# Optimization experiments

Measured on AMD Instinct MI355X. Metric: run time of the kernel, lower is better.

## Reference

```python
import jax, jax.numpy as jnp
import numpy as np

N, T, C = 100000, 12, 32  # nodes, periods, hidden (A3TGCN out_channels hardcoded 32)
E = 3_200_000


def setup_inputs() -> dict:
    key = jax.random.key(0)
    ks = jax.random.split(key, 20)
    s_g = 1.0 / np.sqrt(1.0)        # GCNConv glorot-ish for in=1
    s_l = 1.0 / np.sqrt(2.0 * C)    # torch Linear default for in=2C
    s_h = 1.0 / np.sqrt(C)
    u = lambda k, shape, s: jax.random.uniform(k, shape, jnp.float32, -s, s)
    return {
        "x": jax.random.normal(ks[0], (N, T), jnp.float32),
        "edge_index": jax.random.randint(ks[1], (2, E), 0, N, jnp.int32),
        "edge_weight": jax.random.uniform(ks[2], (E,), jnp.float32),
        # TGCN gate GCNConv params (in_channels=1, out=C)
        "w_z": u(ks[3], (1, C), s_g), "b_z": jnp.zeros((C,), jnp.float32),
        "w_r": u(ks[4], (1, C), s_g), "b_r": jnp.zeros((C,), jnp.float32),
        "w_h": u(ks[5], (1, C), s_g), "b_h": jnp.zeros((C,), jnp.float32),
        # TGCN gate Linear params (torch layout [out=C, in=2C])
        "lw_z": u(ks[6], (C, 2 * C), s_l), "lb_z": u(ks[7], (C,), s_l),
        "lw_r": u(ks[8], (C, 2 * C), s_l), "lb_r": u(ks[9], (C,), s_l),
        "lw_h": u(ks[10], (C, 2 * C), s_l), "lb_h": u(ks[11], (C,), s_l),
        # A3TGCN temporal attention
        "att": jax.random.uniform(ks[12], (T,), jnp.float32),
        # head Linear(32, 1)
        "head_w": u(ks[13], (1, C), s_h), "head_b": u(ks[14], (1,), s_h),
    }


def reference(x, edge_index, edge_weight, w_z, b_z, w_r, b_r, w_h, b_h,
              lw_z, lb_z, lw_r, lb_r, lw_h, lb_h, att, head_w, head_b):
    n = x.shape[0]
    # --- GCN normalization with self-loops (fill value 1) ---
    loop = jnp.arange(n)
    s = jnp.concatenate([edge_index[0], loop])
    d = jnp.concatenate([edge_index[1], loop])
    w = jnp.concatenate([edge_weight, jnp.ones((n,), edge_weight.dtype)])
    deg = jax.ops.segment_sum(w, d, num_segments=n)
    dinv = jnp.where(deg > 0, jax.lax.rsqrt(deg), 0.0)
    norm = dinv[s] * w * dinv[d]
    # --- shared sparse aggregation: A_hat @ X for all periods at once ---
    # in_channels = 1, so GCNConv(X_t) = (A_hat x_t) * W + b; aggregate scalars [N,T]
    agg = jax.ops.segment_sum(norm[:, None] * x[s], d, num_segments=n)  # [N, T]
    # gate convolutions, [N, T, C]
    cz = agg[:, :, None] * w_z[0] + b_z
    ch = agg[:, :, None] * w_h[0] + b_h
    # A3TGCN passes H=None every period -> hidden starts at 0 each step, so
    # linear([conv, H]) reduces to conv @ W[:, :C].T + b, and the reset gate R
    # multiplies H=0 (no effect on output).
    Z = jax.nn.sigmoid(jnp.einsum('ntc,oc->nto', cz, lw_z[:, :C]) + lb_z)
    Ht = jnp.tanh(jnp.einsum('ntc,oc->nto', ch, lw_h[:, :C]) + lb_h)
    Hp = (1.0 - Z) * Ht  # per-period hidden state, [N, T, C]
    probs = jax.nn.softmax(att)
    h = jnp.einsum('t,ntc->nc', probs, Hp)  # attention-weighted temporal sum
    h = jax.nn.relu(h)
    return h @ head_w.T + head_b  # [N, 1]
```

## Files before the change

kernel.cpp:

```cpp
#include <hip/hip_runtime.h>

#define N_NODES 100000
#define T_P 12
#define C_H 32
#define E_EDGES 3200000

#define NODES_PER_B 128
#define NB 782
#define MAX_BE 5120

#define VEC_E (E_EDGES / 4)
#define P1_THREADS 512
#define P1_VECS 2048
#define NBLK1 ((VEC_E + P1_VECS - 1) / P1_VECS)


__global__ void params_kernel(const float* __restrict__ wz, const float* __restrict__ bz,
                              const float* __restrict__ wh, const float* __restrict__ bh,
                              const float* __restrict__ lwz, const float* __restrict__ lbz,
                              const float* __restrict__ lwh, const float* __restrict__ lbh,
                              const float* __restrict__ att, float* __restrict__ P,
                              int* __restrict__ cursor) {
    int o = threadIdx.x;
    if (o < NB) cursor[o] = 0;
    if (o < C_H) {
        float az = 0.f, bzv = 0.f, ah = 0.f, bhv = 0.f;
        for (int c = 0; c < C_H; ++c) {
            float lz = lwz[o * 2 * C_H + c];
            float lh = lwh[o * 2 * C_H + c];
            az += wz[c] * lz;  bzv += bz[c] * lz;
            ah += wh[c] * lh;  bhv += bh[c] * lh;
        }
        P[16 + o]  = az;  P[48 + o]  = bzv + lbz[o];
        P[80 + o]  = ah;  P[112 + o] = bhv + lbh[o];
    }
    if (o == 0) {
        float m = -1e30f;
        for (int t = 0; t < T_P; ++t) m = fmaxf(m, att[t]);
        float e[T_P], s = 0.f;
        for (int t = 0; t < T_P; ++t) { e[t] = __expf(att[t] - m); s += e[t]; }
        float inv = 1.0f / s;
        for (int t = 0; t < T_P; ++t) P[t] = e[t] * inv;
    }
}

__global__ void bucket_scatter_kernel(const int* __restrict__ src, const int* __restrict__ dst,
                                      const float* __restrict__ w, int* __restrict__ cursor,
                                      float2* __restrict__ entries) {
    __shared__ int h[NB];
    __shared__ int claim[NB];
    for (int i = threadIdx.x; i < NB; i += P1_THREADS) h[i] = 0;
    __syncthreads();
    const int4* d4 = (const int4*)dst;
    int vbase = blockIdx.x * P1_VECS;
    int4 dc[4];
    int4 rk[4];
#pragma unroll
    for (int k = 0; k < 4; ++k) {
        int v = vbase + threadIdx.x + k * P1_THREADS;
        if (v < VEC_E) {
            int4 d = d4[v];
            dc[k] = d;
            rk[k].x = atomicAdd(&h[d.x >> 7], 1);
            rk[k].y = atomicAdd(&h[d.y >> 7], 1);
            rk[k].z = atomicAdd(&h[d.z >> 7], 1);
            rk[k].w = atomicAdd(&h[d.w >> 7], 1);
        }
    }
    __syncthreads();
    for (int i = threadIdx.x; i < NB; i += P1_THREADS) {
        int c = h[i];
        claim[i] = c ? atomicAdd(&cursor[i], c) : 0;
    }
    __syncthreads();
    const int4* s4 = (const int4*)src;
    const float4* w4 = (const float4*)w;
#pragma unroll
    for (int k = 0; k < 4; ++k) {
        int v = vbase + threadIdx.x + k * P1_THREADS;
        if (v < VEC_E) {
            int4 s = s4[v];
            float4 ww = w4[v];
            int4 d = dc[k];
            int bin, dl, pos;
            bin = d.x >> 7; dl = d.x & 127;
            pos = bin * MAX_BE + claim[bin] + rk[k].x;
            entries[pos] = make_float2(__int_as_float(s.x | (dl << 17)), ww.x);
            bin = d.y >> 7; dl = d.y & 127;
            pos = bin * MAX_BE + claim[bin] + rk[k].y;
            entries[pos] = make_float2(__int_as_float(s.y | (dl << 17)), ww.y);
            bin = d.z >> 7; dl = d.z & 127;
            pos = bin * MAX_BE + claim[bin] + rk[k].z;
            entries[pos] = make_float2(__int_as_float(s.z | (dl << 17)), ww.z);
            bin = d.w >> 7; dl = d.w & 127;
            pos = bin * MAX_BE + claim[bin] + rk[k].w;
            entries[pos] = make_float2(__int_as_float(s.w | (dl << 17)), ww.w);
        }
    }
}

__global__ void __launch_bounds__(1024)
reorder_kernel(float2* __restrict__ entries, const int* __restrict__ cursor,
               int* __restrict__ node_off, int* __restrict__ node_end,
               float* __restrict__ dinv) {
    __shared__ float2 stage[MAX_BE];
    __shared__ int   cnt[NODES_PER_B];
    __shared__ float wsum[NODES_PER_B];
    __shared__ int   off[NODES_PER_B];
    __shared__ int   rnk[NODES_PER_B];
    int tid = threadIdx.x;
    int b = blockIdx.x;
    int lo = b * MAX_BE;
    int ne = cursor[b];
    if (ne > MAX_BE) ne = MAX_BE;
    if (tid < NODES_PER_B) { cnt[tid] = 0; wsum[tid] = 0.f; }
    __syncthreads();
    for (int k = tid; k < ne; k += 1024) {
        float2 e = entries[lo + k];
        stage[k] = e;
        int dl = (__float_as_int(e.x) >> 17) & 127;
        atomicAdd(&cnt[dl], 1);
        atomicAdd(&wsum[dl], e.y);
    }
    __syncthreads();
    if (tid < NODES_PER_B) off[tid] = cnt[tid];
    __syncthreads();
    for (int d = 1; d < NODES_PER_B; d <<= 1) {
        int t = (tid >= d && tid < NODES_PER_B) ? off[tid - d] : 0;
        __syncthreads();
        if (tid < NODES_PER_B) off[tid] += t;
        __syncthreads();
    }
    if (tid < NODES_PER_B) {
        int ex = off[tid] - cnt[tid];
        rnk[tid] = ex;
        int n = (b << 7) + tid;
        if (n < N_NODES) {
            node_off[n] = lo + ex;
            node_end[n] = lo + ex + cnt[tid];
            dinv[n] = rsqrtf(1.0f + wsum[tid]);
        }
    }
    __syncthreads();
    for (int k = tid; k < ne; k += 1024) {
        float2 e = stage[k];
        int u = __float_as_int(e.x);
        int dl = (u >> 17) & 127;
        int s = u & 0x1FFFF;
        int r = atomicAdd(&rnk[dl], 1);
        entries[lo + r] = make_float2(__int_as_float(s), e.y);
    }
}

__global__ void y_kernel(const float* __restrict__ x, const float* __restrict__ dinv,
                         float* __restrict__ y) {
    int n = blockIdx.x * blockDim.x + threadIdx.x;
    if (n >= N_NODES) return;
    float din = dinv[n];
    const float4* xn = (const float4*)(x + (size_t)n * T_P);
    float4 a0 = xn[0], a1 = xn[1], a2 = xn[2];
    a0.x *= din; a0.y *= din; a0.z *= din; a0.w *= din;
    a1.x *= din; a1.y *= din; a1.z *= din; a1.w *= din;
    a2.x *= din; a2.y *= din; a2.z *= din; a2.w *= din;
    float4* yn = (float4*)(y + ((size_t)n << 4));
    yn[0] = a0; yn[1] = a1; yn[2] = a2;
    yn[3] = make_float4(0.f, 0.f, 0.f, 0.f);
}

__global__ void __launch_bounds__(512, 8)
gather_final_kernel(const int* __restrict__ node_off, const int* __restrict__ node_end,
                    const float2* __restrict__ entries, const float* __restrict__ dinv,
                    const float* __restrict__ y, const float* __restrict__ P,
                    const float* __restrict__ head_w, const float* __restrict__ head_b,
                    float* __restrict__ out) {
    __shared__ float Ps[160];
    __shared__ float hws[32];
    if (threadIdx.x < 160) Ps[threadIdx.x] = P[threadIdx.x];
    if (threadIdx.x < 32) hws[threadIdx.x] = head_w[threadIdx.x];
    __syncthreads();
    int tid = blockIdx.x * blockDim.x + threadIdx.x;
    int n = tid >> 2;
    int lane = tid & 3;
    if (n >= N_NODES) return;
    int b = node_off[n], e = node_end[n];
    const float4* yn = (const float4*)(y + ((size_t)n << 4));
    float4 a0 = make_float4(0.f, 0.f, 0.f, 0.f);
    float4 a1 = a0, a2 = a0;
    if (lane == 0)      a0 = yn[0];
    else if (lane == 1) a1 = yn[1];
    else if (lane == 2) a2 = yn[2];
    for (int i = b + lane; i < e; i += 4) {
        float2 ent = entries[i];
        int s = __float_as_int(ent.x);
        float c = ent.y;
        const float4* ys = (const float4*)(y + ((size_t)s << 4));
        float4 s0 = ys[0], s1 = ys[1], s2 = ys[2];
        a0.x += c * s0.x; a0.y += c * s0.y; a0.z += c * s0.z; a0.w += c * s0.w;
        a1.x += c * s1.x; a1.y += c * s1.y; a1.z += c * s1.z; a1.w += c * s1.w;
        a2.x += c * s2.x; a2.y += c * s2.y; a2.z += c * s2.z; a2.w += c * s2.w;
    }
#define RED4(v) v += __shfl_xor(v, 1); v += __shfl_xor(v, 2)
    RED4(a0.x); RED4(a0.y); RED4(a0.z); RED4(a0.w);
    RED4(a1.x); RED4(a1.y); RED4(a1.z); RED4(a1.w);
    RED4(a2.x); RED4(a2.y); RED4(a2.z); RED4(a2.w);
#undef RED4
    float din = dinv[n];
    float av[T_P];
    av[0] = a0.x * din; av[1] = a0.y * din; av[2]  = a0.z * din; av[3]  = a0.w * din;
    av[4] = a1.x * din; av[5] = a1.y * din; av[6]  = a1.z * din; av[7]  = a1.w * din;
    av[8] = a2.x * din; av[9] = a2.y * din; av[10] = a2.z * din; av[11] = a2.w * din;
    float acc = 0.f;
#pragma unroll
    for (int k = 0; k < 8; ++k) {
        int c = (lane << 3) + k;
        float Az = Ps[16 + c], Bz = Ps[48 + c], Ah = Ps[80 + c], Bh = Ps[112 + c];
        float hc = 0.f;
#pragma unroll
        for (int t = 0; t < T_P; ++t) {
            float a = av[t];
            float oz = 1.f / (1.f + __expf(a * Az + Bz));
            float vv = a * Ah + Bh;
            float th = 1.f - 2.f / (1.f + __expf(2.f * vv));
            hc += Ps[t] * oz * th;
        }
        acc += fmaxf(hc, 0.f) * hws[c];
    }
    acc += __shfl_xor(acc, 1);
    acc += __shfl_xor(acc, 2);
    if (lane == 0) out[n] = acc + head_b[0];
}

extern "C" void kernel_launch(void* const* d_in, const int* in_sizes, int n_in,
                              void* d_out, int out_size, void* d_ws, size_t ws_size,
                              hipStream_t stream) {
    const float* x    = (const float*)d_in[0];
    const int*   ei   = (const int*)d_in[1];
    const float* ew   = (const float*)d_in[2];
    const float* w_z  = (const float*)d_in[3];
    const float* b_z  = (const float*)d_in[4];
    const float* w_h  = (const float*)d_in[7];
    const float* b_h  = (const float*)d_in[8];
    const float* lw_z = (const float*)d_in[9];
    const float* lb_z = (const float*)d_in[10];
    const float* lw_h = (const float*)d_in[13];
    const float* lb_h = (const float*)d_in[14];
    const float* att  = (const float*)d_in[15];
    const float* hw   = (const float*)d_in[16];
    const float* hb   = (const float*)d_in[17];
    float* out = (float*)d_out;

    float* wsf      = (float*)d_ws;
    float* P        = wsf;
    float* dinv     = P + 256;
    int*   cursor   = (int*)(dinv + N_NODES);
    int*   node_off = cursor + NB;
    int*   node_end = node_off + N_NODES;
    float* y        = wsf + 301040;
    float2* entries = (float2*)(y + (size_t)N_NODES * 16);

    const int* srcp = ei;
    const int* dstp = ei + E_EDGES;

    params_kernel<<<1, 1024, 0, stream>>>(w_z, b_z, w_h, b_h, lw_z, lb_z, lw_h, lb_h,
                                          att, P, cursor);
    bucket_scatter_kernel<<<NBLK1, P1_THREADS, 0, stream>>>(srcp, dstp, ew, cursor, entries);
    reorder_kernel<<<NB, 1024, 0, stream>>>(entries, cursor, node_off, node_end, dinv);
    y_kernel<<<(N_NODES + 255) / 256, 256, 0, stream>>>(x, dinv, y);
    gather_final_kernel<<<(N_NODES * 4 + 511) / 512, 512, 0, stream>>>(
        node_off, node_end, entries, dinv, y, P, hw, hb, out);
}
```

Before: 271.4 us.

## Fuse per-bucket sort into gather kernel and split out degree pass

The reorder kernel, which sorted bucket entries by destination and wrote them back to global memory along with node offsets, is removed. A light degree kernel now only sums edge weights per node to compute dinv. The gather kernel sorts each bucket in shared memory as a 16-bit index permutation and aggregates straight from the staged entries, avoiding the global write-back and re-read of entries and the node_off/node_end arrays. Bucket capacity is reduced and scatter writes are bounds-checked, so a bucket larger than the capacity would silently drop edges. Since the gather now runs one 512-thread block per bucket with about 40 KB of shared memory, occupancy may fall.

```diff
diff --git a/kernel.cpp b/kernel.cpp
--- a/kernel.cpp
+++ b/kernel.cpp
@@ -7,7 +7,7 @@
 
 #define NODES_PER_B 128
 #define NB 782
-#define MAX_BE 5120
+#define MAX_BE 4608
 
 #define VEC_E (E_EDGES / 4)
 #define P1_THREADS 512
@@ -84,71 +84,39 @@
             int4 d = dc[k];
             int bin, dl, pos;
             bin = d.x >> 7; dl = d.x & 127;
-            pos = bin * MAX_BE + claim[bin] + rk[k].x;
-            entries[pos] = make_float2(__int_as_float(s.x | (dl << 17)), ww.x);
+            pos = claim[bin] + rk[k].x;
+            if (pos < MAX_BE) entries[bin * MAX_BE + pos] = make_float2(__int_as_float(s.x | (dl << 17)), ww.x);
             bin = d.y >> 7; dl = d.y & 127;
-            pos = bin * MAX_BE + claim[bin] + rk[k].y;
-            entries[pos] = make_float2(__int_as_float(s.y | (dl << 17)), ww.y);
+            pos = claim[bin] + rk[k].y;
+            if (pos < MAX_BE) entries[bin * MAX_BE + pos] = make_float2(__int_as_float(s.y | (dl << 17)), ww.y);
             bin = d.z >> 7; dl = d.z & 127;
-            pos = bin * MAX_BE + claim[bin] + rk[k].z;
-            entries[pos] = make_float2(__int_as_float(s.z | (dl << 17)), ww.z);
+            pos = claim[bin] + rk[k].z;
+            if (pos < MAX_BE) entries[bin * MAX_BE + pos] = make_float2(__int_as_float(s.z | (dl << 17)), ww.z);
             bin = d.w >> 7; dl = d.w & 127;
-            pos = bin * MAX_BE + claim[bin] + rk[k].w;
-            entries[pos] = make_float2(__int_as_float(s.w | (dl << 17)), ww.w);
-        }
-    }
-}
-
-__global__ void __launch_bounds__(1024)
-reorder_kernel(float2* __restrict__ entries, const int* __restrict__ cursor,
-               int* __restrict__ node_off, int* __restrict__ node_end,
-               float* __restrict__ dinv) {
-    __shared__ float2 stage[MAX_BE];
-    __shared__ int   cnt[NODES_PER_B];
+            pos = claim[bin] + rk[k].w;
+            if (pos < MAX_BE) entries[bin * MAX_BE + pos] = make_float2(__int_as_float(s.w | (dl << 17)), ww.w);
+        }
+    }
+}
+
+__global__ void __launch_bounds__(512)
+degree_kernel(const float2* __restrict__ entries, const int* __restrict__ cursor,
+              float* __restrict__ dinv) {
     __shared__ float wsum[NODES_PER_B];
-    __shared__ int   off[NODES_PER_B];
-    __shared__ int   rnk[NODES_PER_B];
     int tid = threadIdx.x;
     int b = blockIdx.x;
     int lo = b * MAX_BE;
-    int ne = cursor[b];
-    if (ne > MAX_BE) ne = MAX_BE;
-    if (tid < NODES_PER_B) { cnt[tid] = 0; wsum[tid] = 0.f; }
-    __syncthreads();
-    for (int k = tid; k < ne; k += 1024) {
+    int ne = cursor[b]; if (ne > MAX_BE) ne = MAX_BE;
+    if (tid < NODES_PER_B) wsum[tid] = 0.f;
+    __syncthreads();
+    for (int k = tid; k < ne; k += 512) {
         float2 e = entries[lo + k];
-        stage[k] = e;
-        int dl = (__float_as_int(e.x) >> 17) & 127;
-        atomicAdd(&cnt[dl], 1);
-        atomicAdd(&wsum[dl], e.y);
-    }
-    __syncthreads();
-    if (tid < NODES_PER_B) off[tid] = cnt[tid];
-    __syncthreads();
-    for (int d = 1; d < NODES_PER_B; d <<= 1) {
-        int t = (tid >= d && tid < NODES_PER_B) ? off[tid - d] : 0;
-        __syncthreads();
-        if (tid < NODES_PER_B) off[tid] += t;
-        __syncthreads();
-    }
+        atomicAdd(&wsum[(__float_as_int(e.x) >> 17) & 127], e.y);
+    }
+    __syncthreads();
     if (tid < NODES_PER_B) {
-        int ex = off[tid] - cnt[tid];
-        rnk[tid] = ex;
         int n = (b << 7) + tid;
-        if (n < N_NODES) {
-            node_off[n] = lo + ex;
-            node_end[n] = lo + ex + cnt[tid];
-            dinv[n] = rsqrtf(1.0f + wsum[tid]);
-        }
-    }
-    __syncthreads();
-    for (int k = tid; k < ne; k += 1024) {
-        float2 e = stage[k];
-        int u = __float_as_int(e.x);
-        int dl = (u >> 17) & 127;
-        int s = u & 0x1FFFF;
-        int r = atomicAdd(&rnk[dl], 1);
-        entries[lo + r] = make_float2(__int_as_float(s), e.y);
+        if (n < N_NODES) dinv[n] = rsqrtf(1.0f + wsum[tid]);
     }
 }
 
@@ -167,31 +135,62 @@
     yn[3] = make_float4(0.f, 0.f, 0.f, 0.f);
 }
 
-__global__ void __launch_bounds__(512, 8)
-gather_final_kernel(const int* __restrict__ node_off, const int* __restrict__ node_end,
-                    const float2* __restrict__ entries, const float* __restrict__ dinv,
-                    const float* __restrict__ y, const float* __restrict__ P,
-                    const float* __restrict__ head_w, const float* __restrict__ head_b,
-                    float* __restrict__ out) {
+__global__ void __launch_bounds__(512)
+sort_gather_kernel(const float2* __restrict__ entries, const int* __restrict__ cursor,
+                   const float* __restrict__ dinv, const float* __restrict__ y,
+                   const float* __restrict__ P, const float* __restrict__ head_w,
+                   const float* __restrict__ head_b, float* __restrict__ out) {
+    __shared__ float2 stage[MAX_BE];
+    __shared__ unsigned short sidx[MAX_BE];
+    __shared__ int   cnt[NODES_PER_B];
+    __shared__ int   inc[NODES_PER_B];
+    __shared__ int   rnk[NODES_PER_B];
     __shared__ float Ps[160];
-    __shared__ float hws[32];
-    if (threadIdx.x < 160) Ps[threadIdx.x] = P[threadIdx.x];
-    if (threadIdx.x < 32) hws[threadIdx.x] = head_w[threadIdx.x];
-    __syncthreads();
-    int tid = blockIdx.x * blockDim.x + threadIdx.x;
-    int n = tid >> 2;
-    int lane = tid & 3;
+    __shared__ float hws[C_H];
+    int tid = threadIdx.x;
+    int b = blockIdx.x;
+    int lo = b * MAX_BE;
+    int ne = cursor[b]; if (ne > MAX_BE) ne = MAX_BE;
+    if (tid < 160) Ps[tid] = P[tid];
+    if (tid < C_H) hws[tid] = head_w[tid];
+    if (tid < NODES_PER_B) cnt[tid] = 0;
+    __syncthreads();
+    for (int k = tid; k < ne; k += 512) {
+        float2 e = entries[lo + k];
+        stage[k] = e;
+        atomicAdd(&cnt[(__float_as_int(e.x) >> 17) & 127], 1);
+    }
+    __syncthreads();
+    if (tid < NODES_PER_B) inc[tid] = cnt[tid];
+    __syncthreads();
+    for (int d = 1; d < NODES_PER_B; d <<= 1) {
+        int t = (tid >= d && tid < NODES_PER_B) ? inc[tid - d] : 0;
+        __syncthreads();
+        if (tid < NODES_PER_B) inc[tid] += t;
+        __syncthreads();
+    }
+    if (tid < NODES_PER_B) rnk[tid] = inc[tid] - cnt[tid];
+    __syncthreads();
+    for (int k = tid; k < ne; k += 512) {
+        int dl = (__float_as_int(stage[k].x) >> 17) & 127;
+        int r = atomicAdd(&rnk[dl], 1);
+        sidx[r] = (unsigned short)k;
+    }
+    __syncthreads();
+    int nl = tid >> 2, lane = tid & 3;
+    int n = (b << 7) + nl;
     if (n >= N_NODES) return;
-    int b = node_off[n], e = node_end[n];
+    int end = inc[nl];
+    int start = end - cnt[nl];
     const float4* yn = (const float4*)(y + ((size_t)n << 4));
     float4 a0 = make_float4(0.f, 0.f, 0.f, 0.f);
     float4 a1 = a0, a2 = a0;
     if (lane == 0)      a0 = yn[0];
     else if (lane == 1) a1 = yn[1];
     else if (lane == 2) a2 = yn[2];
-    for (int i = b + lane; i < e; i += 4) {
-        float2 ent = entries[i];
-        int s = __float_as_int(ent.x);
+    for (int j = start + lane; j < end; j += 4) {
+        float2 ent = stage[sidx[j]];
+        int s = __float_as_int(ent.x) & 0x1FFFF;
         float c = ent.y;
         const float4* ys = (const float4*)(y + ((size_t)s << 4));
         float4 s0 = ys[0], s1 = ys[1], s2 = ys[2];
@@ -253,9 +252,7 @@
     float* P        = wsf;
     float* dinv     = P + 256;
     int*   cursor   = (int*)(dinv + N_NODES);
-    int*   node_off = cursor + NB;
-    int*   node_end = node_off + N_NODES;
-    float* y        = wsf + 301040;
+    float* y        = wsf + 101040;
     float2* entries = (float2*)(y + (size_t)N_NODES * 16);
 
     const int* srcp = ei;
@@ -264,8 +261,7 @@
     params_kernel<<<1, 1024, 0, stream>>>(w_z, b_z, w_h, b_h, lw_z, lb_z, lw_h, lb_h,
                                           att, P, cursor);
     bucket_scatter_kernel<<<NBLK1, P1_THREADS, 0, stream>>>(srcp, dstp, ew, cursor, entries);
-    reorder_kernel<<<NB, 1024, 0, stream>>>(entries, cursor, node_off, node_end, dinv);
+    degree_kernel<<<NB, 512, 0, stream>>>(entries, cursor, dinv);
     y_kernel<<<(N_NODES + 255) / 256, 256, 0, stream>>>(x, dinv, y);
-    gather_final_kernel<<<(N_NODES * 4 + 511) / 512, 512, 0, stream>>>(
-        node_off, node_end, entries, dinv, y, P, hw, hb, out);
-}
+    sort_gather_kernel<<<NB, 512, 0, stream>>>(entries, cursor, dinv, y, P, hw, hb, out);
+}
```

After: 253.6 us. 6.6% less time.
